# Optimization experiments

Hardware: AMD Instinct MI355X
Metric: run time of the kernel (lower is better)

## Reference

```python
import jax, jax.numpy as jnp
import numpy as np

SR = 22050.0  # samplerate; nyquist = SR/2


def _conv1d(x, w, b, pad):
    # x: [B, Cin, T], w: [Cout, Cin, K]
    y = jax.lax.conv_general_dilated(x, w, (1,), [(pad, pad)],
                                     dimension_numbers=('NCH', 'OIH', 'NCH'))
    return y + b[None, :, None]


def _lrelu(x):
    return jnp.where(x >= 0, x, 0.2 * x)


def _lin_upsample(x, factor):
    # torch F.upsample(mode='linear', align_corners=False) ~ half-pixel linear resize
    B, C, T = x.shape
    return jax.image.resize(x, (B, C, T * factor), method='linear')


def _oscillator_bank(f, a, sr):
    # f, a: [B, n_osc, T] -> audio [B, T]
    f = jnp.clip(f, 20.0, sr / 2.0)
    phase = jnp.cumsum(f * (2.0 * np.pi / sr), axis=-1)  # cumulative phase integration
    return jnp.sum(jnp.sin(phase) * a, axis=1)


def _noise_bank2(mags, noise):
    # mags: [B, n_coeffs, n_frames] rfft magnitudes per frame; noise: [B, total_samples]
    B, n_coeffs, n_frames = mags.shape
    window = (n_coeffs - 1) * 2
    hop = window // 2
    total = hop * n_frames
    padded = jnp.pad(noise, ((0, 0), (0, hop)))           # [B, total + hop]
    blocks = padded.reshape(B, n_frames + 1, hop)
    frames = jnp.concatenate([blocks[:, :-1], blocks[:, 1:]], axis=-1)  # [B, n_frames, window]
    spec = jnp.fft.rfft(frames, axis=-1)                   # [B, n_frames, n_coeffs]
    spec = spec * mags.transpose(0, 2, 1)                  # filter white noise per frame
    filt = jnp.fft.irfft(spec, n=window, axis=-1)          # (torch normalized rfft/irfft scales cancel)
    out = jnp.zeros((B, hop * (n_frames + 1)), filt.dtype)
    out = out.at[:, :n_frames * hop].add(filt[..., :hop].reshape(B, -1))
    out = out.at[:, hop:].add(filt[..., hop:].reshape(B, -1))
    return out[:, :total].reshape(B, 1, total)


def _forward(x, noise, mw0, mb0, mw1, mb1, mw2, mb2, mw3, mb3, fw, fb,
             gw0, gb0, gw1, gb1, gw2, gb2, gw3, gb3, lw, lb,
             nw0, nb0, nw1, nb1, nw2, nb2, nw3, nb3, nlw, nlb):
    B, _, T = x.shape
    up = noise.shape[1] // T  # upsample_factor = output_size // input_size
    n_osc = fw.shape[0]

    # oscillator frequency ranges (constants, as in __init__)
    stops = np.geomspace(20.0, SR / 2.0, num=n_osc)
    diffs = np.diff(np.concatenate([[0.0], stops]))
    starts = jnp.asarray(stops - diffs, jnp.float32)[None, :, None]
    diffs_j = jnp.asarray(diffs, jnp.float32)[None, :, None]

    # loudness path (main2 -> loudness ** 2)
    h = x
    for w_, b_ in ((gw0, gb0), (gw1, gb1), (gw2, gb2), (gw3, gb3)):
        h = _lrelu(_conv1d(h, w_, b_, 1))
    loud = _conv1d(h, lw, lb, 1) ** 2  # [B, n_osc, T]

    # frequency path (main -> sigmoid -> map to [start, stop])
    h = x
    for w_, b_ in ((mw0, mb0), (mw1, mb1), (mw2, mb2), (mw3, mb3)):
        h = _lrelu(_conv1d(h, w_, b_, 1))
    f = starts + jax.nn.sigmoid(_conv1d(h, fw, fb, 1)) * diffs_j  # [B, n_osc, T]

    h = x
    for w_, b_ in ((nw0, nb0), (nw1, nb1), (nw2, nb2), (nw3, nb3)):
        h = jnp.repeat(h, 2, axis=-1)
        h = _lrelu(_conv1d(h, w_, b_, 3))
    n_l = _conv1d(h, nlw, nlb, 1) ** 2  # [B, 17, 1024]

    loud = _lin_upsample(loud, up)  # [B, n_osc, output_size]
    f = _lin_upsample(f, up)
    harmonic = _oscillator_bank(f, loud, SR).reshape(B, 1, -1)
    return harmonic + _noise_bank2(n_l, noise)


def setup_inputs() -> dict:
    key = jax.random.key(0)
    ks = jax.random.split(key, 40)
    B, Cin, T, c, n_osc, out_size = 16, 128, 64, 512, 128, 16384
    n_coeffs = out_size // 1024 + 1  # 17
    inp = {}
    inp['x'] = jax.random.normal(ks[0], (B, Cin, T), jnp.float32)
    inp['noise'] = jax.random.uniform(ks[1], (B, out_size), jnp.float32, minval=-1.0, maxval=1.0)
    specs = [('mw0', c, Cin, 3), ('mw1', c, c, 3), ('mw2', c, c, 3), ('mw3', c, c, 3), ('fw', n_osc, c, 3),
             ('gw0', c, Cin, 3), ('gw1', c, c, 3), ('gw2', c, c, 3), ('gw3', c, c, 3), ('lw', n_osc, c, 3),
             ('nw0', c, Cin, 7), ('nw1', c, c, 7), ('nw2', c, c, 7), ('nw3', c, c, 7), ('nlw', n_coeffs, c, 3)]
    for j, (nm, o, i, ksz) in enumerate(specs):
        kw, kb = jax.random.split(ks[2 + j])
        inp[nm] = jax.random.normal(kw, (o, i, ksz), jnp.float32) * (1.0 / np.sqrt(i * ksz))
        inp[nm.replace('w', 'b', 1)] = jax.random.normal(kb, (o,), jnp.float32) * 0.01
    return inp


def reference(x, noise, mw0, mb0, mw1, mb1, mw2, mb2, mw3, mb3, fw, fb,
              gw0, gb0, gw1, gb1, gw2, gb2, gw3, gb3, lw, lb,
              nw0, nb0, nw1, nb1, nw2, nb2, nw3, nb3, nlw, nlb):
    return _forward(x, noise, mw0, mb0, mw1, mb1, mw2, mb2, mw3, mb3, fw, fb,
                    gw0, gb0, gw1, gb1, gw2, gb2, gw3, gb3, lw, lb,
                    nw0, nb0, nw1, nb1, nw2, nb2, nw3, nb3, nlw, nlb)
```

## Files before the change

kernel.cpp:

```cpp
#include <hip/hip_runtime.h>
#include <math.h>

#define ACT_LRELU  0
#define ACT_SIGMAP 1
#define ACT_SQUARE 2

typedef __attribute__((ext_vector_type(8))) short v8s;
typedef __attribute__((ext_vector_type(4))) short v4s;
typedef __attribute__((ext_vector_type(16))) float f32x16;

static __device__ __forceinline__ float lrelu(float x) { return x >= 0.f ? x : 0.2f * x; }

static __device__ __forceinline__ short bf16rne(float x) {
  unsigned u = __float_as_uint(x);
  unsigned r = (u + 0x7FFFu + ((u >> 16) & 1u)) >> 16;
  return (short)r;
}
static __device__ __forceinline__ float bf16tof(short h) {
  return __uint_as_float(((unsigned)(unsigned short)h) << 16);
}
static __device__ __forceinline__ void split3(float v, short& h, short& l, short& q) {
  h = bf16rne(v); float r1 = v - bf16tof(h);
  l = bf16rne(r1); float r2 = r1 - bf16tof(l);
  q = bf16rne(r2);
}

__global__ void __launch_bounds__(256) prep_acts(
    const float* __restrict__ x, short* __restrict__ xm3)
{
  int e = blockIdx.x * 256 + threadIdx.x;
  if (e >= 131072) return;
  int b = e >> 13, rem = e & 8191, t = rem >> 7, ci = rem & 127;
  float v = x[((size_t)(b * 128) + ci) * 64 + t];
  short h, l, q; split3(v, h, l, q);
  size_t o = ((size_t)(b * 64) + t) * 128 + ci;
  xm3[0 * 131072 + o] = h;
  xm3[1 * 131072 + o] = l;
  xm3[2 * 131072 + o] = q;
}

__global__ void __launch_bounds__(256) prep_panels(
    const float* mw0, const float* mw1, const float* mw2, const float* mw3, const float* fw,
    const float* gw0, const float* gw1, const float* gw2, const float* gw3, const float* lw,
    short* __restrict__ mP, short* __restrict__ gP)
{
  int i = blockIdx.x * 256 + threadIdx.x;
  const int PER = 114688;
  if (i >= 2 * PER) return;
  int path = i >= PER ? 1 : 0;
  int r = i - path * PER;
  int layer, Cin, Cout; size_t poff;
  if (r < 8192)        { layer = 0;              Cin = 128; Cout = 512; poff = 0; }
  else if (r < 40960)  { layer = 1; r -= 8192;   Cin = 512; Cout = 512; poff = 589824; }
  else if (r < 73728)  { layer = 2; r -= 40960;  Cin = 512; Cout = 512; poff = 2949120; }
  else if (r < 106496) { layer = 3; r -= 73728;  Cin = 512; Cout = 512; poff = 5308416; }
  else                 { layer = 4; r -= 106496; Cin = 512; Cout = 128; poff = 7667712; }
  const float* Wm[5] = {mw0, mw1, mw2, mw3, fw};
  const float* Wg[5] = {gw0, gw1, gw2, gw3, lw};
  const float* W = path ? Wg[layer] : Wm[layer];
  short* P = (path ? gP : mP) + poff;
  const int nci8 = Cin >> 3;
  int co = r / nci8, ci = (r - co * nci8) * 8;
  const int K3 = 3 * Cin;
  const float* wp = W + (size_t)(co * Cin + ci) * 3;
  v8s hv[3], lv[3], qv[3];
#pragma unroll
  for (int j = 0; j < 8; ++j)
#pragma unroll
    for (int tap = 0; tap < 3; ++tap) {
      short h, l, q; split3(wp[j * 3 + tap], h, l, q);
      hv[tap][j] = h; lv[tap][j] = l; qv[tap][j] = q;
    }
#pragma unroll
  for (int tap = 0; tap < 3; ++tap) {
    size_t base = (size_t)co * K3 + tap * Cin + ci;
    *(v8s*)&P[(size_t)0 * Cout * K3 + base] = hv[tap];
    *(v8s*)&P[(size_t)1 * Cout * K3 + base] = lv[tap];
    *(v8s*)&P[(size_t)2 * Cout * K3 + base] = qv[tap];
  }
}

__global__ void __launch_bounds__(128, 2) conv_path_tap(
    const short* __restrict__ actM, const short* __restrict__ actG,
    const short* __restrict__ Pm, const short* __restrict__ Pg,
    float* __restrict__ partial, int Cin, int Cout, int psIn)
{
  const int mtiles = Cout >> 6;
  const int nblk = 2 * mtiles * 16 * 3;
  const int Q = nblk >> 3;
  int d = blockIdx.x;
  int idx = (d & 7) * Q + (d >> 3);
  int mt = idx % mtiles; int r = idx / mtiles;
  int nt = r & 15; r >>= 4;
  int tap = r % 3; int path = r / 3;

  const short* act = path ? actG : actM;
  const short* P   = path ? Pg : Pm;
  const int K3 = 3 * Cin;
  const int co0 = mt * 64;
  const int NT  = Cin >> 5;
  const int npl = path ? 2 : 3;

  const int tid = threadIdx.x;
  const int w = tid >> 6;
  const int l = tid & 63;

  __shared__ __align__(16) short Al[3][64 * 40];
  __shared__ __align__(16) short Bl[3][64 * 40];

  f32x16 acc[2] = {};
  v8s rA[3][2], rB[3][2];

  auto LOADA = [&](int t) {
    int ci0 = t << 5;
#pragma unroll
    for (int pl = 0; pl < 3; ++pl)
      if (pl < npl)
#pragma unroll
        for (int it = 0; it < 2; ++it) {
          int e = it * 128 + tid;
          int row = e >> 2, c8 = e & 3;
          rA[pl][it] = *(const v8s*)&P[(size_t)pl * Cout * K3 + (size_t)(co0 + row) * K3
                                       + tap * Cin + ci0 + c8 * 8];
        }
  };
  auto LOADB = [&](int t) {
    int ci0 = t << 5;
#pragma unroll
    for (int pl = 0; pl < 3; ++pl)
      if (pl < npl)
#pragma unroll
        for (int it = 0; it < 2; ++it) {
          int e = it * 128 + tid;
          int n = e >> 2, c8 = e & 3;
          int trow = n + tap - 1;
          v8s vv = {};
          if (trow >= 0 && trow < 64)
            vv = *(const v8s*)&act[(size_t)pl * psIn + ((size_t)(nt * 64 + trow)) * Cin
                                   + ci0 + c8 * 8];
          rB[pl][it] = vv;
        }
  };
  auto WRITE = [&]() {
#pragma unroll
    for (int pl = 0; pl < 3; ++pl)
      if (pl < npl)
#pragma unroll
        for (int it = 0; it < 2; ++it) {
          int e = it * 128 + tid;
          *(v8s*)&Al[pl][(e >> 2) * 40 + (e & 3) * 8] = rA[pl][it];
          *(v8s*)&Bl[pl][(e >> 2) * 40 + (e & 3) * 8] = rB[pl][it];
        }
  };

  LOADA(0); LOADB(0);
  WRITE();
  __syncthreads();

  for (int t = 0; t < NT; ++t) {
    if (t + 1 < NT) { LOADA(t + 1); LOADB(t + 1); }
    const int lr = l & 31, lh = (l >> 5) * 8;
#pragma unroll
    for (int kk = 0; kk < 2; ++kk) {
      const int ao = (w * 32 + lr) * 40 + kk * 16 + lh;
      v8s a0 = *(const v8s*)&Al[0][ao];
      v8s a1 = *(const v8s*)&Al[1][ao];
#pragma unroll
      for (int fn = 0; fn < 2; ++fn) {
        const int bo = (fn * 32 + lr) * 40 + kk * 16 + lh;
        v8s b0 = *(const v8s*)&Bl[0][bo];
        v8s b1 = *(const v8s*)&Bl[1][bo];
        acc[fn] = __builtin_amdgcn_mfma_f32_32x32x16_bf16(a0, b0, acc[fn], 0, 0, 0);
        acc[fn] = __builtin_amdgcn_mfma_f32_32x32x16_bf16(a0, b1, acc[fn], 0, 0, 0);
        acc[fn] = __builtin_amdgcn_mfma_f32_32x32x16_bf16(a1, b0, acc[fn], 0, 0, 0);
        if (path == 0) {
          v8s a2 = *(const v8s*)&Al[2][ao];
          v8s b2 = *(const v8s*)&Bl[2][bo];
          acc[fn] = __builtin_amdgcn_mfma_f32_32x32x16_bf16(a1, b1, acc[fn], 0, 0, 0);
          acc[fn] = __builtin_amdgcn_mfma_f32_32x32x16_bf16(a0, b2, acc[fn], 0, 0, 0);
          acc[fn] = __builtin_amdgcn_mfma_f32_32x32x16_bf16(a2, b0, acc[fn], 0, 0, 0);
        }
      }
    }
    __syncthreads();
    if (t + 1 < NT) { WRITE(); __syncthreads(); }
  }

  const int hi4 = 4 * (l >> 5);
  const size_t pbase = (size_t)(tap * 2 + path) * 1024;
#pragma unroll
  for (int fn = 0; fn < 2; ++fn) {
    int gn = nt * 64 + fn * 32 + (l & 31);
#pragma unroll
    for (int q4 = 0; q4 < 4; ++q4) {
      int co = co0 + w * 32 + q4 * 8 + hi4;
      float4 v = {acc[fn][q4 * 4 + 0], acc[fn][q4 * 4 + 1],
                  acc[fn][q4 * 4 + 2], acc[fn][q4 * 4 + 3]};
      *(float4*)&partial[(pbase + gn) * Cout + co] = v;
    }
  }
}

__global__ void __launch_bounds__(256) finalize_lrelu(
    const float* __restrict__ partial,
    const float* __restrict__ BsM, const float* __restrict__ BsG,
    short* __restrict__ soutM, short* __restrict__ soutG)
{
  int e = blockIdx.x * 256 + threadIdx.x;
  int c4 = e & 127, gn = (e >> 7) & 1023, path = e >> 17;
  const float* Bs = path ? BsG : BsM;
  short* sout = path ? soutG : soutM;
  size_t base = ((size_t)(path) * 1024 + gn) * 512 + c4 * 4;
  const size_t TS = (size_t)2 * 1024 * 512;
  float4 s0 = *(const float4*)&partial[base];
  float4 s1 = *(const float4*)&partial[base + TS];
  float4 s2 = *(const float4*)&partial[base + 2 * TS];
  float4 bi = *(const float4*)&Bs[c4 * 4];
  const float* p0 = &s0.x; const float* p1 = &s1.x;
  const float* p2 = &s2.x; const float* pb = &bi.x;
  v4s h4, l4, q4v;
#pragma unroll
  for (int j = 0; j < 4; ++j) {
    float z = lrelu(p0[j] + p1[j] + p2[j] + pb[j]);
    short h, lo, qq; split3(z, h, lo, qq);
    h4[j] = h; l4[j] = lo; q4v[j] = qq;
  }
  size_t o = (size_t)gn * 512 + c4 * 4;
  *(v4s*)&sout[0 * 524288 + o] = h4;
  *(v4s*)&sout[1 * 524288 + o] = l4;
  *(v4s*)&sout[2 * 524288 + o] = q4v;
}

__global__ void __launch_bounds__(256) finalize_l5(
    const float* __restrict__ partial,
    const float* __restrict__ fb, const float* __restrict__ lb,
    float* __restrict__ fsm, float* __restrict__ lsm)
{
  __shared__ float bandS[2][128];
  int tid = threadIdx.x;
  if (tid < 128) {
    double lg = log(551.25);
    double stop  = 20.0 * exp(lg * (double)tid / 127.0);
    double start = (tid == 0) ? 0.0 : 20.0 * exp(lg * (double)(tid - 1) / 127.0);
    bandS[0][tid] = (float)start;
    bandS[1][tid] = (float)(stop - start);
  }
  __syncthreads();

  int e = blockIdx.x * 256 + tid;
  int c4 = e & 31, gn = (e >> 5) & 1023, path = e >> 15;
  size_t base = ((size_t)(path) * 1024 + gn) * 128 + c4 * 4;
  const size_t TS = (size_t)2 * 1024 * 128;
  float4 s0 = *(const float4*)&partial[base];
  float4 s1 = *(const float4*)&partial[base + TS];
  float4 s2 = *(const float4*)&partial[base + 2 * TS];
  float4 bi = *(const float4*)&((path ? lb : fb)[c4 * 4]);
  const float* p0 = &s0.x; const float* p1 = &s1.x;
  const float* p2 = &s2.x; const float* pb = &bi.x;
  int b = gn >> 6, t = gn & 63;
#pragma unroll
  for (int j = 0; j < 4; ++j) {
    int co = c4 * 4 + j;
    float z = p0[j] + p1[j] + p2[j] + pb[j];
    if (path == 0)
      fsm[((size_t)(b * 128) + co) * 64 + t] = bandS[0][co] + bandS[1][co] / (1.f + expf(-z));
    else
      lsm[((size_t)(b * 128) + co) * 64 + t] = z * z;
  }
}

__global__ void __launch_bounds__(256) fold_all(
    const float* __restrict__ nw0, const float* __restrict__ nw1,
    const float* __restrict__ nw2, const float* __restrict__ nw3,
    const float* __restrict__ nlw,
    short* __restrict__ E1, short* __restrict__ E2,
    short* __restrict__ E3, short* __restrict__ E4,
    short* __restrict__ Pnl)
{
  int i = blockIdx.x * 256 + threadIdx.x;
  if (i >= 106496) {
    if (i >= 108544) return;
    int idx = i - 106496;
    int co = idx >> 6, ci = (idx & 63) * 8;
    v8s hv[3], lv[3];
#pragma unroll
    for (int j = 0; j < 8; ++j)
#pragma unroll
      for (int tap = 0; tap < 3; ++tap) {
        float v = (co < 17) ? nlw[((size_t)(co * 512 + ci + j)) * 3 + tap] : 0.f;
        short h = bf16rne(v);
        hv[tap][j] = h;
        lv[tap][j] = bf16rne(v - bf16tof(h));
      }
#pragma unroll
    for (int tap = 0; tap < 3; ++tap) {
      *(v8s*)&Pnl[(size_t)(0 * 32 + co) * 1536 + tap * 512 + ci] = hv[tap];
      *(v8s*)&Pnl[(size_t)(1 * 32 + co) * 1536 + tap * 512 + ci] = lv[tap];
    }
    return;
  }
  const float* W; short* Ag; int Cin; int idx;
  if (i < 8192)        { W = nw0; Ag = E1; Cin = 128; idx = i; }
  else if (i < 40960)  { W = nw1; Ag = E2; Cin = 512; idx = i - 8192; }
  else if (i < 73728)  { W = nw2; Ag = E3; Cin = 512; idx = i - 40960; }
  else                 { W = nw3; Ag = E4; Cin = 512; idx = i - 73728; }
  const int nci8 = Cin >> 3;
  int co = idx / nci8, ci = (idx - co * nci8) * 8;
  const float* wp = W + (size_t)(co * Cin + ci) * 7;
  const int K = Cin * 4;
  v8s he[4], le[4], ho[4], lo4[4];
#pragma unroll
  for (int j = 0; j < 8; ++j) {
    const float* w = wp + j * 7;
    float fe[4] = {w[0],        w[1] + w[2], w[3] + w[4], w[5] + w[6]};
    float fo[4] = {w[0] + w[1], w[2] + w[3], w[4] + w[5], w[6]};
#pragma unroll
    for (int q = 0; q < 4; ++q) {
      short h1 = bf16rne(fe[q]);
      he[q][j] = h1; le[q][j] = bf16rne(fe[q] - bf16tof(h1));
      short h2 = bf16rne(fo[q]);
      ho[q][j] = h2; lo4[q][j] = bf16rne(fo[q] - bf16tof(h2));
    }
  }
#pragma unroll
  for (int q = 0; q < 4; ++q) {
    size_t kbase = (size_t)q * Cin + ci;
    *(v8s*)&Ag[((size_t)(0 * 512 + co)) * K + kbase] = he[q];
    *(v8s*)&Ag[((size_t)(1 * 512 + co)) * K + kbase] = le[q];
    *(v8s*)&Ag[((size_t)(2 * 512 + co)) * K + kbase] = ho[q];
    *(v8s*)&Ag[((size_t)(3 * 512 + co)) * K + kbase] = lo4[q];
  }
}

template<int MF, int BNS, int CIN>
__global__ void __launch_bounds__(256, 2) conv_noise(
    const short* __restrict__ actIn, const short* __restrict__ Ag,
    const float* __restrict__ Bs, short* __restrict__ actOut,
    int Sin, int psIn, int psOut)
{
  constexpr int NF   = BNS / 64;
  constexpr int BM   = MF * 64;
  constexpr int AITS = BM / 32;
  constexpr int SLAB = BNS + 3;
  constexpr int BSL  = (2 * SLAB * 8 + 255) / 256;
  constexpr int K    = CIN * 4;
  constexpr int nci  = CIN / 64;
  const int mtiles = 512 / BM;
  const int stiles = Sin / BNS;
  const int nblk = mtiles * 2 * 16 * stiles;
  const int Q = nblk >> 3;
  int d = blockIdx.x;
  int idx = (d & 7) * Q + (d >> 3);
  int mt = idx % mtiles;
  int t1 = idx / mtiles;
  int par = t1 & 1;
  int rest = t1 >> 1;
  int st = rest % stiles;
  int b = rest / stiles;

  const int co0 = mt * BM;
  const int s0 = st * BNS;
  const int soff = par ? -1 : -2;

  const int tid = threadIdx.x;
  const int w = tid >> 6, wm = w & 1, wn = w >> 1;
  const int l = tid & 63;

  __shared__ __align__(16) short Al[2][BM * 72];
  __shared__ __align__(16) short Bl[2][SLAB * 72];

  f32x16 acc[MF][NF] = {};
  v8s rA[2][AITS];
  v8s rBS[BSL];

  auto LOADA = [&](int q, int ci0) {
#pragma unroll
    for (int pl = 0; pl < 2; ++pl)
#pragma unroll
      for (int it = 0; it < AITS; ++it) {
        int e = it * 256 + tid;
        int row = e >> 3, c8 = e & 7;
        rA[pl][it] = *(const v8s*)&Ag[((size_t)((par * 2 + pl) * 512 + co0 + row)) * K
                                      + q * CIN + ci0 + c8 * 8];
      }
  };
  auto WRITEA = [&]() {
#pragma unroll
    for (int pl = 0; pl < 2; ++pl)
#pragma unroll
      for (int it = 0; it < AITS; ++it) {
        int e = it * 256 + tid;
        *(v8s*)&Al[pl][(e >> 3) * 72 + (e & 7) * 8] = rA[pl][it];
      }
  };
  auto LOADBS = [&](int ci0) {
#pragma unroll
    for (int it = 0; it < BSL; ++it) {
      int e = it * 256 + tid;
      v8s vv = {};
      if (e < 2 * SLAB * 8) {
        int r3 = e >> 3, c8 = e & 7;
        int pl = r3 / SLAB, row = r3 - pl * SLAB;
        int srow = s0 + soff + row;
        if (srow >= 0 && srow < Sin)
          vv = *(const v8s*)&actIn[(size_t)pl * psIn + ((size_t)(b * Sin + srow)) * CIN
                                   + ci0 + c8 * 8];
      }
      rBS[it] = vv;
    }
  };
  auto WRITEBS = [&]() {
#pragma unroll
    for (int it = 0; it < BSL; ++it) {
      int e = it * 256 + tid;
      if (e < 2 * SLAB * 8) {
        int r3 = e >> 3, c8 = e & 7;
        int pl = r3 / SLAB, row = r3 - pl * SLAB;
        *(v8s*)&Bl[pl][row * 72 + c8 * 8] = rBS[it];
      }
    }
  };

  LOADBS(0); LOADA(0, 0);
  WRITEBS(); WRITEA();
  __syncthreads();

  for (int ci = 0; ci < nci; ++ci) {
    const int ci0 = ci << 6;
#pragma unroll
    for (int q = 0; q < 4; ++q) {
      const bool lastq = (q == 3);
      const bool lastall = lastq && (ci == nci - 1);
      if (!lastq)        LOADA(q + 1, ci0);
      else if (!lastall) { LOADBS(ci0 + 64); LOADA(0, ci0 + 64); }

      const int lr = l & 31, lh = (l >> 5) * 8;
#pragma unroll
      for (int kk = 0; kk < 4; ++kk) {
        v8s ah[MF], al[MF], bh[NF], bl[NF];
#pragma unroll
        for (int fm = 0; fm < MF; ++fm) {
          int ab = (wm * (MF * 32) + fm * 32 + lr) * 72 + kk * 16 + lh;
          ah[fm] = *(const v8s*)&Al[0][ab];
          al[fm] = *(const v8s*)&Al[1][ab];
        }
#pragma unroll
        for (int fn = 0; fn < NF; ++fn) {
          int bb = (wn * (BNS / 2) + fn * 32 + lr + q) * 72 + kk * 16 + lh;
          bh[fn] = *(const v8s*)&Bl[0][bb];
          bl[fn] = *(const v8s*)&Bl[1][bb];
        }
#pragma unroll
        for (int fm = 0; fm < MF; ++fm)
#pragma unroll
          for (int fn = 0; fn < NF; ++fn) {
            acc[fm][fn] = __builtin_amdgcn_mfma_f32_32x32x16_bf16(ah[fm], bh[fn], acc[fm][fn], 0, 0, 0);
            acc[fm][fn] = __builtin_amdgcn_mfma_f32_32x32x16_bf16(ah[fm], bl[fn], acc[fm][fn], 0, 0, 0);
            acc[fm][fn] = __builtin_amdgcn_mfma_f32_32x32x16_bf16(al[fm], bh[fn], acc[fm][fn], 0, 0, 0);
          }
      }
      __syncthreads();
      if (!lastall) {
        if (!lastq) WRITEA();
        else { WRITEBS(); WRITEA(); }
        __syncthreads();
      }
    }
  }

  const int hi4 = 4 * (l >> 5);
  const int T2 = 2 * Sin;
#pragma unroll
  for (int fm = 0; fm < MF; ++fm)
#pragma unroll
    for (int q4 = 0; q4 < 4; ++q4) {
      int co = co0 + wm * (MF * 32) + fm * 32 + q4 * 8 + hi4;
      float4 bia = *(const float4*)&Bs[co];
      const float* bp = &bia.x;
#pragma unroll
      for (int fn = 0; fn < NF; ++fn) {
        int s_l = wn * (BNS / 2) + fn * 32 + (l & 31);
        int t = 2 * (s0 + s_l) + par;
        v4s h4, l4;
#pragma unroll
        for (int j = 0; j < 4; ++j) {
          float z = lrelu(acc[fm][fn][q4 * 4 + j] + bp[j]);
          short h = bf16rne(z);
          h4[j] = h;
          l4[j] = bf16rne(z - bf16tof(h));
        }
        size_t o = ((size_t)(b * T2) + t) * 512 + co;
        *(v4s*)&actOut[0 * (size_t)psOut + o] = h4;
        *(v4s*)&actOut[1 * (size_t)psOut + o] = l4;
      }
    }
}

#define NL_PS4 8388608

__global__ void __launch_bounds__(128) conv_nl_filter(
    const short* __restrict__ act, const short* __restrict__ Pnl,
    const float* __restrict__ Bs, const float* __restrict__ noise,
    float* __restrict__ filt)
{
  const int bid = blockIdx.x;
  const int b = bid >> 4, t0 = (bid & 15) << 6;
  const int tid = threadIdx.x;
  const int w = tid >> 6;
  const int l = tid & 63;

  __shared__ __align__(16) short Al[2 * 3 * 32 * 72];
  __shared__ __align__(16) short Bl[2 * 66 * 72];
  __shared__ float magS[64][20];
  __shared__ float ctS[32], stS[32];

  if (tid < 32) {
    double a = (double)tid * (3.14159265358979323846 / 16.0);
    ctS[tid] = (float)cos(a);
    stS[tid] = (float)sin(a);
  }

  f32x16 acc = {};

  for (int ci0 = 0; ci0 < 512; ci0 += 64) {
    for (int e = tid; e < 1536; e += 128) {
      int c8 = e & 7, row = e >> 3;
      int pl = row >= 96;
      int r2 = row - pl * 96;
      int tap = r2 >> 5, co = r2 & 31;
      v8s vv = *(const v8s*)&Pnl[(size_t)(pl * 32 + co) * 1536 + tap * 512 + ci0 + c8 * 8];
      *(v8s*)&Al[row * 72 + c8 * 8] = vv;
    }
    for (int e = tid; e < 1056; e += 128) {
      int c8 = e & 7, r = (e >> 3) % 66, pl = (e >> 3) / 66;
      int t = t0 + r - 1;
      v8s vv = {};
      if (t >= 0 && t < 1024)
        vv = *(const v8s*)&act[(size_t)pl * NL_PS4 + ((size_t)(b << 10) + t) * 512 + ci0 + c8 * 8];
      *(v8s*)&Bl[(pl * 66 + r) * 72 + c8 * 8] = vv;
    }
    __syncthreads();
    const int lr = l & 31, lh = (l >> 5) * 8;
#pragma unroll
    for (int kk = 0; kk < 4; ++kk)
#pragma unroll
      for (int tap = 0; tap < 3; ++tap) {
        v8s a_h = *(const v8s*)&Al[((0 * 3 + tap) * 32 + lr) * 72 + kk * 16 + lh];
        v8s a_l = *(const v8s*)&Al[((1 * 3 + tap) * 32 + lr) * 72 + kk * 16 + lh];
        int brow = w * 32 + lr + tap;
        v8s b_h = *(const v8s*)&Bl[(0 * 66 + brow) * 72 + kk * 16 + lh];
        v8s b_l = *(const v8s*)&Bl[(1 * 66 + brow) * 72 + kk * 16 + lh];
        acc = __builtin_amdgcn_mfma_f32_32x32x16_bf16(a_h, b_h, acc, 0, 0, 0);
        acc = __builtin_amdgcn_mfma_f32_32x32x16_bf16(a_h, b_l, acc, 0, 0, 0);
        acc = __builtin_amdgcn_mfma_f32_32x32x16_bf16(a_l, b_h, acc, 0, 0, 0);
      }
    __syncthreads();
  }

  const int t_loc = w * 32 + (l & 31);
  const int hi4 = 4 * (l >> 5);
#pragma unroll
  for (int q4 = 0; q4 < 4; ++q4)
#pragma unroll
    for (int j = 0; j < 4; ++j) {
      int co = q4 * 8 + hi4 + j;
      if (co < 17) {
        float z = acc[q4 * 4 + j] + Bs[co];
        magS[t_loc][co] = z * z;
      }
    }
  __syncthreads();

  if (tid < 64) {
    int i = t0 + tid;
    float xv[32];
#pragma unroll
    for (int n = 0; n < 32; ++n) {
      int idx = i * 16 + n;
      xv[n] = (idx < 16384) ? noise[(size_t)b * 16384 + idx] : 0.f;
    }
    float Yr[17], Yi[17];
#pragma unroll
    for (int k = 0; k <= 16; ++k) {
      float xr = 0.f, xi = 0.f;
      int kk = 0;
#pragma unroll
      for (int n = 0; n < 32; ++n) {
        xr += xv[n] * ctS[kk];
        xi -= xv[n] * stS[kk];
        kk = (kk + k) & 31;
      }
      float m = magS[tid][k];
      Yr[k] = xr * m;
      Yi[k] = xi * m;
    }
    float* fo = filt + ((size_t)(b << 10) + i) * 32;
#pragma unroll
    for (int n = 0; n < 32; ++n) {
      float v = Yr[0] + ((n & 1) ? -Yr[16] : Yr[16]);
      int kk = n;
#pragma unroll
      for (int k = 1; k <= 15; ++k) {
        v += 2.f * (Yr[k] * ctS[kk] - Yi[k] * stS[kk]);
        kk = (kk + n) & 31;
      }
      fo[n] = v * (1.f / 32.f);
    }
  }
}

static __device__ __forceinline__ int clamp64(int i) { return i < 0 ? 0 : (i > 63 ? 63 : i); }

__global__ void __launch_bounds__(256) osc_phase(
    const float* __restrict__ fsm, double* __restrict__ phaseBase)
{
  const int o = blockIdx.x, b = blockIdx.y;
  const float* frow = fsm + (size_t)(b * 128 + o) * 64;
  const int c = threadIdx.x;

  const float ic0 = ((float)(c * 64) - 127.5f) * (1.0f / 256.0f);
  const int ilo = (int)floorf(ic0);
  float f0 = frow[clamp64(ilo)], f1 = frow[clamp64(ilo + 1)], f2 = frow[clamp64(ilo + 2)];

  double local = 0.0;
#pragma unroll 8
  for (int j = 0; j < 64; ++j) {
    float ic = ic0 + (float)j * (1.0f / 256.0f);
    float fl = floorf(ic);
    float w  = ic - fl;
    bool hi = ((int)fl) > ilo;
    float fa = hi ? f1 : f0;
    float fb = hi ? f2 : f1;
    float f = fa * (1.f - w) + fb * w;
    f = fminf(fmaxf(f, 20.f), 11025.f);
    local += (double)f;
  }
  local *= (1.0 / 22050.0);

  __shared__ double ps[256];
  ps[c] = local;
  __syncthreads();
  for (int off = 1; off < 256; off <<= 1) {
    double v = (c >= off) ? ps[c - off] : 0.0;
    __syncthreads();
    ps[c] += v;
    __syncthreads();
  }
  phaseBase[(size_t)(b * 128 + o) * 256 + c] = ps[c] - local;
}

__global__ void __launch_bounds__(128) osc_sum(
    const float* __restrict__ fsm, const float* __restrict__ lsm,
    const double* __restrict__ phaseBase, const float* __restrict__ filt,
    float* __restrict__ out)
{
  const int c = blockIdx.x, b = blockIdx.y;
  const int tid = threadIdx.x;
  __shared__ float contrib[128][65];
  __shared__ float part[2][64];
  const int o = tid;
  const float* frow = fsm + (size_t)(b * 128 + o) * 64;
  const float* arow = lsm + (size_t)(b * 128 + o) * 64;

  double pb = phaseBase[(size_t)(b * 128 + o) * 256 + c];
  float fb0 = (float)(pb - floor(pb));

  const float ic0 = ((float)(c * 64) - 127.5f) * (1.0f / 256.0f);
  const int ilo = (int)floorf(ic0);
  float f0 = frow[clamp64(ilo)], f1 = frow[clamp64(ilo + 1)], f2 = frow[clamp64(ilo + 2)];
  float a0 = arow[clamp64(ilo)], a1 = arow[clamp64(ilo + 1)], a2 = arow[clamp64(ilo + 2)];

  float rel = 0.f, comp = 0.f;
#pragma unroll 8
  for (int j = 0; j < 64; ++j) {
    float ic = ic0 + (float)j * (1.0f / 256.0f);
    float fl = floorf(ic);
    float w  = ic - fl;
    bool hi = ((int)fl) > ilo;
    float fa = hi ? f1 : f0;
    float fb = hi ? f2 : f1;
    float f = fa * (1.f - w) + fb * w;
    f = fminf(fmaxf(f, 20.f), 11025.f);
    float y = f * (1.0f / 22050.0f) - comp;
    float t = rel + y;
    comp = (t - rel) - y;
    rel = t;
    float tot = fb0 + rel;
    float frac = tot - floorf(tot);
    float s = sinpif(2.f * frac);
    float aa = hi ? a1 : a0;
    float ab = hi ? a2 : a1;
    float am = aa * (1.f - w) + ab * w;
    contrib[o][j] = s * am;
  }
  __syncthreads();
  int half = tid >> 6, tl = tid & 63;
  float sum = 0.f;
  for (int oo = 0; oo < 64; ++oo) sum += contrib[half * 64 + oo][tl];
  part[half][tl] = sum;
  __syncthreads();
  if (tid < 64) {
    int t = c * 64 + tid;
    float v = part[0][tid] + part[1][tid];
    int i0 = t >> 4, r = t & 15;
    v += filt[((size_t)(b << 10) + i0) * 32 + r];
    if (i0 > 0) v += filt[((size_t)(b << 10) + i0 - 1) * 32 + 16 + r];
    out[(size_t)b * 16384 + t] = v;
  }
}

extern "C" void kernel_launch(void* const* d_in, const int* in_sizes, int n_in,
                              void* d_out, int out_size, void* d_ws, size_t ws_size,
                              hipStream_t stream)
{
  (void)in_sizes; (void)n_in; (void)out_size; (void)ws_size;

  const float* x     = (const float*)d_in[0];
  const float* noise = (const float*)d_in[1];
  const float* mw0 = (const float*)d_in[2];  const float* mb0 = (const float*)d_in[3];
  const float* mw1 = (const float*)d_in[4];  const float* mb1 = (const float*)d_in[5];
  const float* mw2 = (const float*)d_in[6];  const float* mb2 = (const float*)d_in[7];
  const float* mw3 = (const float*)d_in[8];  const float* mb3 = (const float*)d_in[9];
  const float* fw  = (const float*)d_in[10]; const float* fb  = (const float*)d_in[11];
  const float* gw0 = (const float*)d_in[12]; const float* gb0 = (const float*)d_in[13];
  const float* gw1 = (const float*)d_in[14]; const float* gb1 = (const float*)d_in[15];
  const float* gw2 = (const float*)d_in[16]; const float* gb2 = (const float*)d_in[17];
  const float* gw3 = (const float*)d_in[18]; const float* gb3 = (const float*)d_in[19];
  const float* lw  = (const float*)d_in[20]; const float* lb  = (const float*)d_in[21];
  const float* nw0 = (const float*)d_in[22]; const float* nb0 = (const float*)d_in[23];
  const float* nw1 = (const float*)d_in[24]; const float* nb1 = (const float*)d_in[25];
  const float* nw2 = (const float*)d_in[26]; const float* nb2 = (const float*)d_in[27];
  const float* nw3 = (const float*)d_in[28]; const float* nb3 = (const float*)d_in[29];
  const float* nlw = (const float*)d_in[30]; const float* nlb = (const float*)d_in[31];

  char* W8 = (char*)d_ws;
  short* mP  = (short*)(W8 + 0);
  short* gP  = (short*)(W8 + 16515072);
  short* hm0 = (short*)(W8 + 33030144);
  short* hm1 = (short*)(W8 + 36175872);
  short* hg0 = (short*)(W8 + 39321600);
  short* hg1 = (short*)(W8 + 42467328);
  float* partial = (float*)(W8 + 45613056);
  short* xm3 = (short*)(W8 + 58720256);
  float* fsm = (float*)(W8 + 59506688);
  float* lsm = (float*)(W8 + 60030976);
  short* Pnl = (short*)(W8 + 60555264);

  short* E4  = (short*)(W8 + 0);
  short* E3  = (short*)(W8 + 33554432);
  short* E2  = (short*)(W8 + 41943040);
  short* E1  = (short*)(W8 + 50331648);
  short* l1out = (short*)(W8 + 52428800);
  short* l2out = (short*)(W8 + 25165824);
  short* l3out = (short*)(W8 + 8388608);
  short* l4act = (short*)(W8 + 25165824);

  float* filt = (float*)(W8 + 1114112);
  double* phaseBase = (double*)(W8 + 4194304);

  float* out = (float*)d_out;

  const int PS_X = 131072;
  const int PS_H = 524288;

  prep_acts<<<512, 256, 0, stream>>>(x, xm3);
  prep_panels<<<896, 256, 0, stream>>>(mw0, mw1, mw2, mw3, fw,
                                       gw0, gw1, gw2, gw3, lw, mP, gP);

  conv_path_tap<<<768, 128, 0, stream>>>(xm3, xm3, mP + 0, gP + 0, partial, 128, 512, PS_X);
  finalize_lrelu<<<1024, 256, 0, stream>>>(partial, mb0, gb0, hm0, hg0);
  conv_path_tap<<<768, 128, 0, stream>>>(hm0, hg0, mP + 589824, gP + 589824, partial, 512, 512, PS_H);
  finalize_lrelu<<<1024, 256, 0, stream>>>(partial, mb1, gb1, hm1, hg1);
  conv_path_tap<<<768, 128, 0, stream>>>(hm1, hg1, mP + 2949120, gP + 2949120, partial, 512, 512, PS_H);
  finalize_lrelu<<<1024, 256, 0, stream>>>(partial, mb2, gb2, hm0, hg0);
  conv_path_tap<<<768, 128, 0, stream>>>(hm0, hg0, mP + 5308416, gP + 5308416, partial, 512, 512, PS_H);
  finalize_lrelu<<<1024, 256, 0, stream>>>(partial, mb3, gb3, hm1, hg1);
  conv_path_tap<<<192, 128, 0, stream>>>(hm1, hg1, mP + 7667712, gP + 7667712, partial, 512, 128, PS_H);
  finalize_l5<<<256, 256, 0, stream>>>(partial, fb, lb, fsm, lsm);

  fold_all<<<424, 256, 0, stream>>>(nw0, nw1, nw2, nw3, nlw, E1, E2, E3, E4, Pnl);
  conv_noise<1, 64, 128><<<256, 256, 0, stream>>>(xm3, E1, nb0, l1out, 64, PS_X, 1048576);
  conv_noise<2, 64, 512><<<256, 256, 0, stream>>>(l1out, E2, nb1, l2out, 128, 1048576, 2097152);
  conv_noise<2, 128, 512><<<256, 256, 0, stream>>>(l2out, E3, nb2, l3out, 256, 2097152, 4194304);
  conv_noise<2, 128, 512><<<512, 256, 0, stream>>>(l3out, E4, nb3, l4act, 512, 4194304, 8388608);

  conv_nl_filter<<<256, 128, 0, stream>>>(l4act, Pnl, nlb, noise, filt);

  osc_phase<<<dim3(128, 16), 256, 0, stream>>>(fsm, phaseBase);
  osc_sum<<<dim3(256, 16), 128, 0, stream>>>(fsm, lsm, phaseBase, filt, out);
}
```

Before: 514.9 us.

## Fuse conv taps with bias/activation epilogue and merge prep kernels

Replaces the per-tap split-K conv kernel plus separate finalize kernels with a single conv_path kernel that loops over all three taps inside the K loop and applies bias, activation and bf16 split directly in the epilogue. This removes the fp32 partial buffer round-trip and five finalize launches. It also merges the activation and weight prep kernels into one launch and uses 64-wide K tiles with 4 waves. The cost is far fewer blocks per launch (256 or 64 instead of 768 or 192), which lowers parallelism on a large GPU, and the G path now always does all 6 MFMAs on 3 planes instead of 3 on 2.

```diff
diff --git a/kernel.cpp b/kernel.cpp
--- a/kernel.cpp
+++ b/kernel.cpp
@@ -25,39 +25,46 @@
   q = bf16rne(r2);
 }
 
-__global__ void __launch_bounds__(256) prep_acts(
-    const float* __restrict__ x, short* __restrict__ xm3)
-{
-  int e = blockIdx.x * 256 + threadIdx.x;
-  if (e >= 131072) return;
-  int b = e >> 13, rem = e & 8191, t = rem >> 7, ci = rem & 127;
-  float v = x[((size_t)(b * 128) + ci) * 64 + t];
-  short h, l, q; split3(v, h, l, q);
-  size_t o = ((size_t)(b * 64) + t) * 128 + ci;
-  xm3[0 * 131072 + o] = h;
-  xm3[1 * 131072 + o] = l;
-  xm3[2 * 131072 + o] = q;
-}
-
-__global__ void __launch_bounds__(256) prep_panels(
+__global__ void __launch_bounds__(256) prep_mg(
+    const float* __restrict__ x, short* __restrict__ xm3,
     const float* mw0, const float* mw1, const float* mw2, const float* mw3, const float* fw,
     const float* gw0, const float* gw1, const float* gw2, const float* gw3, const float* lw,
     short* __restrict__ mP, short* __restrict__ gP)
 {
-  int i = blockIdx.x * 256 + threadIdx.x;
+  const int blk = blockIdx.x;
+  const int tid = threadIdx.x;
+
+  if (blk < 512) {
+    int e = blk * 256 + tid;
+    if (e >= 131072) return;
+    int b = e >> 13, rem = e & 8191, t = rem >> 7, ci = rem & 127;
+    float v = x[((size_t)(b * 128) + ci) * 64 + t];
+    short h, l, q; split3(v, h, l, q);
+    size_t o = ((size_t)(b * 64) + t) * 128 + ci;
+    xm3[0 * 131072 + o] = h;
+    xm3[1 * 131072 + o] = l;
+    xm3[2 * 131072 + o] = q;
+    return;
+  }
+
+  int i = (blk - 512) * 256 + tid;
   const int PER = 114688;
   if (i >= 2 * PER) return;
   int path = i >= PER ? 1 : 0;
   int r = i - path * PER;
-  int layer, Cin, Cout; size_t poff;
-  if (r < 8192)        { layer = 0;              Cin = 128; Cout = 512; poff = 0; }
-  else if (r < 40960)  { layer = 1; r -= 8192;   Cin = 512; Cout = 512; poff = 589824; }
-  else if (r < 73728)  { layer = 2; r -= 40960;  Cin = 512; Cout = 512; poff = 2949120; }
-  else if (r < 106496) { layer = 3; r -= 73728;  Cin = 512; Cout = 512; poff = 5308416; }
-  else                 { layer = 4; r -= 106496; Cin = 512; Cout = 128; poff = 7667712; }
-  const float* Wm[5] = {mw0, mw1, mw2, mw3, fw};
-  const float* Wg[5] = {gw0, gw1, gw2, gw3, lw};
-  const float* W = path ? Wg[layer] : Wm[layer];
+  int Cin, Cout; size_t poff;
+  const float* W;
+  {
+    int layer;
+    if (r < 8192)        { layer = 0;              Cin = 128; Cout = 512; poff = 0; }
+    else if (r < 40960)  { layer = 1; r -= 8192;   Cin = 512; Cout = 512; poff = 589824; }
+    else if (r < 73728)  { layer = 2; r -= 40960;  Cin = 512; Cout = 512; poff = 2949120; }
+    else if (r < 106496) { layer = 3; r -= 73728;  Cin = 512; Cout = 512; poff = 5308416; }
+    else                 { layer = 4; r -= 106496; Cin = 512; Cout = 128; poff = 7667712; }
+    const float* Wm[5] = {mw0, mw1, mw2, mw3, fw};
+    const float* Wg[5] = {gw0, gw1, gw2, gw3, lw};
+    W = path ? Wg[layer] : Wm[layer];
+  }
   short* P = (path ? gP : mP) + poff;
   const int nci8 = Cin >> 3;
   int co = r / nci8, ci = (r - co * nci8) * 8;
@@ -77,195 +84,6 @@
     *(v8s*)&P[(size_t)0 * Cout * K3 + base] = hv[tap];
     *(v8s*)&P[(size_t)1 * Cout * K3 + base] = lv[tap];
     *(v8s*)&P[(size_t)2 * Cout * K3 + base] = qv[tap];
-  }
-}
-
-__global__ void __launch_bounds__(128, 2) conv_path_tap(
-    const short* __restrict__ actM, const short* __restrict__ actG,
-    const short* __restrict__ Pm, const short* __restrict__ Pg,
-    float* __restrict__ partial, int Cin, int Cout, int psIn)
-{
-  const int mtiles = Cout >> 6;
-  const int nblk = 2 * mtiles * 16 * 3;
-  const int Q = nblk >> 3;
-  int d = blockIdx.x;
-  int idx = (d & 7) * Q + (d >> 3);
-  int mt = idx % mtiles; int r = idx / mtiles;
-  int nt = r & 15; r >>= 4;
-  int tap = r % 3; int path = r / 3;
-
-  const short* act = path ? actG : actM;
-  const short* P   = path ? Pg : Pm;
-  const int K3 = 3 * Cin;
-  const int co0 = mt * 64;
-  const int NT  = Cin >> 5;
-  const int npl = path ? 2 : 3;
-
-  const int tid = threadIdx.x;
-  const int w = tid >> 6;
-  const int l = tid & 63;
-
-  __shared__ __align__(16) short Al[3][64 * 40];
-  __shared__ __align__(16) short Bl[3][64 * 40];
-
-  f32x16 acc[2] = {};
-  v8s rA[3][2], rB[3][2];
-
-  auto LOADA = [&](int t) {
-    int ci0 = t << 5;
-#pragma unroll
-    for (int pl = 0; pl < 3; ++pl)
-      if (pl < npl)
-#pragma unroll
-        for (int it = 0; it < 2; ++it) {
-          int e = it * 128 + tid;
-          int row = e >> 2, c8 = e & 3;
-          rA[pl][it] = *(const v8s*)&P[(size_t)pl * Cout * K3 + (size_t)(co0 + row) * K3
-                                       + tap * Cin + ci0 + c8 * 8];
-        }
-  };
-  auto LOADB = [&](int t) {
-    int ci0 = t << 5;
-#pragma unroll
-    for (int pl = 0; pl < 3; ++pl)
-      if (pl < npl)
-#pragma unroll
-        for (int it = 0; it < 2; ++it) {
-          int e = it * 128 + tid;
-          int n = e >> 2, c8 = e & 3;
-          int trow = n + tap - 1;
-          v8s vv = {};
-          if (trow >= 0 && trow < 64)
-            vv = *(const v8s*)&act[(size_t)pl * psIn + ((size_t)(nt * 64 + trow)) * Cin
-                                   + ci0 + c8 * 8];
-          rB[pl][it] = vv;
-        }
-  };
-  auto WRITE = [&]() {
-#pragma unroll
-    for (int pl = 0; pl < 3; ++pl)
-      if (pl < npl)
-#pragma unroll
-        for (int it = 0; it < 2; ++it) {
-          int e = it * 128 + tid;
-          *(v8s*)&Al[pl][(e >> 2) * 40 + (e & 3) * 8] = rA[pl][it];
-          *(v8s*)&Bl[pl][(e >> 2) * 40 + (e & 3) * 8] = rB[pl][it];
-        }
-  };
-
-  LOADA(0); LOADB(0);
-  WRITE();
-  __syncthreads();
-
-  for (int t = 0; t < NT; ++t) {
-    if (t + 1 < NT) { LOADA(t + 1); LOADB(t + 1); }
-    const int lr = l & 31, lh = (l >> 5) * 8;
-#pragma unroll
-    for (int kk = 0; kk < 2; ++kk) {
-      const int ao = (w * 32 + lr) * 40 + kk * 16 + lh;
-      v8s a0 = *(const v8s*)&Al[0][ao];
-      v8s a1 = *(const v8s*)&Al[1][ao];
-#pragma unroll
-      for (int fn = 0; fn < 2; ++fn) {
-        const int bo = (fn * 32 + lr) * 40 + kk * 16 + lh;
-        v8s b0 = *(const v8s*)&Bl[0][bo];
-        v8s b1 = *(const v8s*)&Bl[1][bo];
-        acc[fn] = __builtin_amdgcn_mfma_f32_32x32x16_bf16(a0, b0, acc[fn], 0, 0, 0);
-        acc[fn] = __builtin_amdgcn_mfma_f32_32x32x16_bf16(a0, b1, acc[fn], 0, 0, 0);
-        acc[fn] = __builtin_amdgcn_mfma_f32_32x32x16_bf16(a1, b0, acc[fn], 0, 0, 0);
-        if (path == 0) {
-          v8s a2 = *(const v8s*)&Al[2][ao];
-          v8s b2 = *(const v8s*)&Bl[2][bo];
-          acc[fn] = __builtin_amdgcn_mfma_f32_32x32x16_bf16(a1, b1, acc[fn], 0, 0, 0);
-          acc[fn] = __builtin_amdgcn_mfma_f32_32x32x16_bf16(a0, b2, acc[fn], 0, 0, 0);
-          acc[fn] = __builtin_amdgcn_mfma_f32_32x32x16_bf16(a2, b0, acc[fn], 0, 0, 0);
-        }
-      }
-    }
-    __syncthreads();
-    if (t + 1 < NT) { WRITE(); __syncthreads(); }
-  }
-
-  const int hi4 = 4 * (l >> 5);
-  const size_t pbase = (size_t)(tap * 2 + path) * 1024;
-#pragma unroll
-  for (int fn = 0; fn < 2; ++fn) {
-    int gn = nt * 64 + fn * 32 + (l & 31);
-#pragma unroll
-    for (int q4 = 0; q4 < 4; ++q4) {
-      int co = co0 + w * 32 + q4 * 8 + hi4;
-      float4 v = {acc[fn][q4 * 4 + 0], acc[fn][q4 * 4 + 1],
-                  acc[fn][q4 * 4 + 2], acc[fn][q4 * 4 + 3]};
-      *(float4*)&partial[(pbase + gn) * Cout + co] = v;
-    }
-  }
-}
-
-__global__ void __launch_bounds__(256) finalize_lrelu(
-    const float* __restrict__ partial,
-    const float* __restrict__ BsM, const float* __restrict__ BsG,
-    short* __restrict__ soutM, short* __restrict__ soutG)
-{
-  int e = blockIdx.x * 256 + threadIdx.x;
-  int c4 = e & 127, gn = (e >> 7) & 1023, path = e >> 17;
-  const float* Bs = path ? BsG : BsM;
-  short* sout = path ? soutG : soutM;
-  size_t base = ((size_t)(path) * 1024 + gn) * 512 + c4 * 4;
-  const size_t TS = (size_t)2 * 1024 * 512;
-  float4 s0 = *(const float4*)&partial[base];
-  float4 s1 = *(const float4*)&partial[base + TS];
-  float4 s2 = *(const float4*)&partial[base + 2 * TS];
-  float4 bi = *(const float4*)&Bs[c4 * 4];
-  const float* p0 = &s0.x; const float* p1 = &s1.x;
-  const float* p2 = &s2.x; const float* pb = &bi.x;
-  v4s h4, l4, q4v;
-#pragma unroll
-  for (int j = 0; j < 4; ++j) {
-    float z = lrelu(p0[j] + p1[j] + p2[j] + pb[j]);
-    short h, lo, qq; split3(z, h, lo, qq);
-    h4[j] = h; l4[j] = lo; q4v[j] = qq;
-  }
-  size_t o = (size_t)gn * 512 + c4 * 4;
-  *(v4s*)&sout[0 * 524288 + o] = h4;
-  *(v4s*)&sout[1 * 524288 + o] = l4;
-  *(v4s*)&sout[2 * 524288 + o] = q4v;
-}
-
-__global__ void __launch_bounds__(256) finalize_l5(
-    const float* __restrict__ partial,
-    const float* __restrict__ fb, const float* __restrict__ lb,
-    float* __restrict__ fsm, float* __restrict__ lsm)
-{
-  __shared__ float bandS[2][128];
-  int tid = threadIdx.x;
-  if (tid < 128) {
-    double lg = log(551.25);
-    double stop  = 20.0 * exp(lg * (double)tid / 127.0);
-    double start = (tid == 0) ? 0.0 : 20.0 * exp(lg * (double)(tid - 1) / 127.0);
-    bandS[0][tid] = (float)start;
-    bandS[1][tid] = (float)(stop - start);
-  }
-  __syncthreads();
-
-  int e = blockIdx.x * 256 + tid;
-  int c4 = e & 31, gn = (e >> 5) & 1023, path = e >> 15;
-  size_t base = ((size_t)(path) * 1024 + gn) * 128 + c4 * 4;
-  const size_t TS = (size_t)2 * 1024 * 128;
-  float4 s0 = *(const float4*)&partial[base];
-  float4 s1 = *(const float4*)&partial[base + TS];
-  float4 s2 = *(const float4*)&partial[base + 2 * TS];
-  float4 bi = *(const float4*)&((path ? lb : fb)[c4 * 4]);
-  const float* p0 = &s0.x; const float* p1 = &s1.x;
-  const float* p2 = &s2.x; const float* pb = &bi.x;
-  int b = gn >> 6, t = gn & 63;
-#pragma unroll
-  for (int j = 0; j < 4; ++j) {
-    int co = c4 * 4 + j;
-    float z = p0[j] + p1[j] + p2[j] + pb[j];
-    if (path == 0)
-      fsm[((size_t)(b * 128) + co) * 64 + t] = bandS[0][co] + bandS[1][co] / (1.f + expf(-z));
-    else
-      lsm[((size_t)(b * 128) + co) * 64 + t] = z * z;
   }
 }
 
@@ -329,6 +147,160 @@
     *(v8s*)&Ag[((size_t)(1 * 512 + co)) * K + kbase] = le[q];
     *(v8s*)&Ag[((size_t)(2 * 512 + co)) * K + kbase] = ho[q];
     *(v8s*)&Ag[((size_t)(3 * 512 + co)) * K + kbase] = lo4[q];
+  }
+}
+
+__global__ void __launch_bounds__(256, 2) conv_path(
+    const short* __restrict__ actM, const short* __restrict__ actG,
+    const short* __restrict__ Pm, const short* __restrict__ Pg,
+    const float* __restrict__ BsM, const float* __restrict__ BsG,
+    float* __restrict__ foutM, float* __restrict__ foutG,
+    short* __restrict__ soutM, short* __restrict__ soutG,
+    int Cin, int Cout, int psIn, int psOut, int actMk, int actGk)
+{
+  const int mtiles = Cout >> 6;
+  const int nblk = 2 * mtiles * 16;
+  const int Q = nblk >> 3;
+  int d = blockIdx.x;
+  int idx = (d & 7) * Q + (d >> 3);
+  int mt = idx % mtiles;
+  int tmp = idx / mtiles;
+  int nt = tmp & 15;
+  int path = tmp >> 4;
+
+  const short* act = path ? actG : actM;
+  const short* P   = path ? Pg : Pm;
+  const float* Bs  = path ? BsG : BsM;
+  float* fout      = path ? foutG : foutM;
+  short* sout      = path ? soutG : soutM;
+  const int actk   = path ? actGk : actMk;
+
+  const int K3 = 3 * Cin;
+  const int co0 = mt * 64;
+  const int n0  = nt * 64;
+  const int nci = Cin >> 6;
+  const int NT  = 3 * nci;
+
+  const int tid = threadIdx.x;
+  const int w = tid >> 6, wm = w & 1, wn = w >> 1;
+  const int l = tid & 63;
+
+  __shared__ __align__(16) short Al[3][64 * 72];
+  __shared__ __align__(16) short Bl[3][64 * 72];
+  __shared__ float bandS[2][128];
+
+  if (actk == ACT_SIGMAP && tid < 128) {
+    double lg = log(551.25);
+    double stop  = 20.0 * exp(lg * (double)tid / 127.0);
+    double start = (tid == 0) ? 0.0 : 20.0 * exp(lg * (double)(tid - 1) / 127.0);
+    bandS[0][tid] = (float)start;
+    bandS[1][tid] = (float)(stop - start);
+  }
+
+  f32x16 acc = {};
+  v8s rA[3][2], rB[3][2];
+
+  auto LOADA = [&](int t) {
+    int tap = t / nci, ci0 = (t % nci) << 6;
+#pragma unroll
+    for (int pl = 0; pl < 3; ++pl)
+#pragma unroll
+      for (int it = 0; it < 2; ++it) {
+        int e = it * 256 + tid;
+        int row = e >> 3, c8 = e & 7;
+        rA[pl][it] = *(const v8s*)&P[(size_t)pl * Cout * K3 + (size_t)(co0 + row) * K3
+                                     + tap * Cin + ci0 + c8 * 8];
+      }
+  };
+  auto LOADB = [&](int t) {
+    int tap = t / nci, ci0 = (t % nci) << 6;
+#pragma unroll
+    for (int pl = 0; pl < 3; ++pl)
+#pragma unroll
+      for (int it = 0; it < 2; ++it) {
+        int e = it * 256 + tid;
+        int n = e >> 3, c8 = e & 7;
+        int gn = n0 + n, bb = gn >> 6, trow = (gn & 63) + tap - 1;
+        v8s vv = {};
+        if (trow >= 0 && trow < 64)
+          vv = *(const v8s*)&act[(size_t)pl * psIn + ((size_t)(bb * 64 + trow)) * Cin
+                                 + ci0 + c8 * 8];
+        rB[pl][it] = vv;
+      }
+  };
+  auto WRITE = [&]() {
+#pragma unroll
+    for (int pl = 0; pl < 3; ++pl)
+#pragma unroll
+      for (int it = 0; it < 2; ++it) {
+        int e = it * 256 + tid;
+        int row = e >> 3, c8 = e & 7;
+        *(v8s*)&Al[pl][row * 72 + c8 * 8] = rA[pl][it];
+        *(v8s*)&Bl[pl][row * 72 + c8 * 8] = rB[pl][it];
+      }
+  };
+
+  LOADA(0); LOADB(0);
+  WRITE();
+  __syncthreads();
+
+  for (int t = 0; t < NT; ++t) {
+    if (t + 1 < NT) { LOADA(t + 1); LOADB(t + 1); }
+    const int abase = (wm * 32 + (l & 31)) * 72 + (l >> 5) * 8;
+    const int bbase = (wn * 32 + (l & 31)) * 72 + (l >> 5) * 8;
+#pragma unroll
+    for (int kk = 0; kk < 4; ++kk) {
+      v8s a0 = *(const v8s*)&Al[0][abase + kk * 16];
+      v8s a1 = *(const v8s*)&Al[1][abase + kk * 16];
+      v8s a2 = *(const v8s*)&Al[2][abase + kk * 16];
+      v8s b0 = *(const v8s*)&Bl[0][bbase + kk * 16];
+      v8s b1 = *(const v8s*)&Bl[1][bbase + kk * 16];
+      v8s b2 = *(const v8s*)&Bl[2][bbase + kk * 16];
+      acc = __builtin_amdgcn_mfma_f32_32x32x16_bf16(a0, b0, acc, 0, 0, 0);
+      acc = __builtin_amdgcn_mfma_f32_32x32x16_bf16(a0, b1, acc, 0, 0, 0);
+      acc = __builtin_amdgcn_mfma_f32_32x32x16_bf16(a1, b0, acc, 0, 0, 0);
+      acc = __builtin_amdgcn_mfma_f32_32x32x16_bf16(a1, b1, acc, 0, 0, 0);
+      acc = __builtin_amdgcn_mfma_f32_32x32x16_bf16(a0, b2, acc, 0, 0, 0);
+      acc = __builtin_amdgcn_mfma_f32_32x32x16_bf16(a2, b0, acc, 0, 0, 0);
+    }
+    __syncthreads();
+    if (t + 1 < NT) { WRITE(); __syncthreads(); }
+  }
+
+  const int ncol = wn * 32 + (l & 31);
+  const int gn = n0 + ncol, bb = gn >> 6, t = gn & 63;
+  const int hi4 = 4 * (l >> 5);
+#pragma unroll
+  for (int q4 = 0; q4 < 4; ++q4) {
+    int co = co0 + wm * 32 + q4 * 8 + hi4;
+    float4 bia = *(const float4*)&Bs[co];
+    const float* bp = &bia.x;
+    float z[4];
+#pragma unroll
+    for (int j = 0; j < 4; ++j) z[j] = acc[q4 * 4 + j] + bp[j];
+    if (actk == ACT_LRELU) {
+      v4s h4, l4, q4v;
+#pragma unroll
+      for (int j = 0; j < 4; ++j) {
+        float zz = lrelu(z[j]);
+        short h, lo, qq; split3(zz, h, lo, qq);
+        h4[j] = h; l4[j] = lo; q4v[j] = qq;
+      }
+      size_t o = ((size_t)(bb * 64) + t) * Cout + co;
+      *(v4s*)&sout[0 * (size_t)psOut + o] = h4;
+      *(v4s*)&sout[1 * (size_t)psOut + o] = l4;
+      *(v4s*)&sout[2 * (size_t)psOut + o] = q4v;
+    } else if (actk == ACT_SIGMAP) {
+#pragma unroll
+      for (int j = 0; j < 4; ++j) {
+        float f = bandS[0][co + j] + bandS[1][co + j] / (1.f + expf(-z[j]));
+        fout[((size_t)(bb * 128) + co + j) * 64 + t] = f;
+      }
+    } else {
+#pragma unroll
+      for (int j = 0; j < 4; ++j)
+        fout[((size_t)(bb * 128) + co + j) * 64 + t] = z[j] * z[j];
+    }
   }
 }
 
@@ -740,7 +712,6 @@
   short* hm1 = (short*)(W8 + 36175872);
   short* hg0 = (short*)(W8 + 39321600);
   short* hg1 = (short*)(W8 + 42467328);
-  float* partial = (float*)(W8 + 45613056);
   short* xm3 = (short*)(W8 + 58720256);
   float* fsm = (float*)(W8 + 59506688);
   float* lsm = (float*)(W8 + 60030976);
@@ -763,20 +734,19 @@
   const int PS_X = 131072;
   const int PS_H = 524288;
 
-  prep_acts<<<512, 256, 0, stream>>>(x, xm3);
-  prep_panels<<<896, 256, 0, stream>>>(mw0, mw1, mw2, mw3, fw,
-                                       gw0, gw1, gw2, gw3, lw, mP, gP);
-
-  conv_path_tap<<<768, 128, 0, stream>>>(xm3, xm3, mP + 0, gP + 0, partial, 128, 512, PS_X);
-  finalize_lrelu<<<1024, 256, 0, stream>>>(partial, mb0, gb0, hm0, hg0);
-  conv_path_tap<<<768, 128, 0, stream>>>(hm0, hg0, mP + 589824, gP + 589824, partial, 512, 512, PS_H);
-  finalize_lrelu<<<1024, 256, 0, stream>>>(partial, mb1, gb1, hm1, hg1);
-  conv_path_tap<<<768, 128, 0, stream>>>(hm1, hg1, mP + 2949120, gP + 2949120, partial, 512, 512, PS_H);
-  finalize_lrelu<<<1024, 256, 0, stream>>>(partial, mb2, gb2, hm0, hg0);
-  conv_path_tap<<<768, 128, 0, stream>>>(hm0, hg0, mP + 5308416, gP + 5308416, partial, 512, 512, PS_H);
-  finalize_lrelu<<<1024, 256, 0, stream>>>(partial, mb3, gb3, hm1, hg1);
-  conv_path_tap<<<192, 128, 0, stream>>>(hm1, hg1, mP + 7667712, gP + 7667712, partial, 512, 128, PS_H);
-  finalize_l5<<<256, 256, 0, stream>>>(partial, fb, lb, fsm, lsm);
+  prep_mg<<<1408, 256, 0, stream>>>(x, xm3,
+      mw0, mw1, mw2, mw3, fw, gw0, gw1, gw2, gw3, lw, mP, gP);
+
+  conv_path<<<256, 256, 0, stream>>>(xm3, xm3, mP + 0, gP + 0, mb0, gb0,
+      nullptr, nullptr, hm0, hg0, 128, 512, PS_X, PS_H, ACT_LRELU, ACT_LRELU);
+  conv_path<<<256, 256, 0, stream>>>(hm0, hg0, mP + 589824, gP + 589824, mb1, gb1,
+      nullptr, nullptr, hm1, hg1, 512, 512, PS_H, PS_H, ACT_LRELU, ACT_LRELU);
+  conv_path<<<256, 256, 0, stream>>>(hm1, hg1, mP + 2949120, gP + 2949120, mb2, gb2,
+      nullptr, nullptr, hm0, hg0, 512, 512, PS_H, PS_H, ACT_LRELU, ACT_LRELU);
+  conv_path<<<256, 256, 0, stream>>>(hm0, hg0, mP + 5308416, gP + 5308416, mb3, gb3,
+      nullptr, nullptr, hm1, hg1, 512, 512, PS_H, PS_H, ACT_LRELU, ACT_LRELU);
+  conv_path<<<64, 256, 0, stream>>>(hm1, hg1, mP + 7667712, gP + 7667712, fb, lb,
+      fsm, lsm, nullptr, nullptr, 512, 128, PS_H, 0, ACT_SIGMAP, ACT_SQUARE);
 
   fold_all<<<424, 256, 0, stream>>>(nw0, nw1, nw2, nw3, nlw, E1, E2, E3, E4, Pnl);
   conv_noise<1, 64, 128><<<256, 256, 0, stream>>>(xm3, E1, nb0, l1out, 64, PS_X, 1048576);
```

Result: no change. 507.7 us (-1.4%).
